# Optimization experiments

Measured on AMD Instinct MI355X. Metric: run time of the kernel, lower is better.

## Reference

```python
import jax, jax.numpy as jnp
import numpy as np

DILATION_RATE = 4
SEGMENT_SIZE = 512


def setup_inputs() -> dict:
    key = jax.random.key(0)
    x = jax.random.normal(key, (4, 8192, 1024), dtype=jnp.float32)
    return {"x": x}


def reference(x):
    """LongNet-style dilated attention.

    For each offset in range(dilation_rate): take the strided slice
    x[:, offset::r, :], split it into segments of length `segment_size`,
    run full softmax(q k^T / sqrt(d)) v attention inside each segment
    (q=k=v=the slice; attention dim is the full d_model, matching how the
    original feeds [B, n_seg, seg, d_model] to FlashAttention), scatter the
    result back to the strided positions, and average the dilation heads
    (softmax over uniform logits == 1/r weights).

    Since seq_len % (r * segment_size) == 0, the r strided slices tile the
    sequence exactly, so we vectorize over offsets with a single reshape:
    position p = i*r + offset  ->  xr[:, i, offset, :].
    """
    r, seg = DILATION_RATE, SEGMENT_SIZE
    B, S, D = x.shape
    n = S // r            # tokens per strided slice
    g = n // seg          # segments per slice
    scale = 1.0 / jnp.sqrt(jnp.asarray(D, dtype=x.dtype))

    xs = x.reshape(B, g, seg, r, D)  # [B, g, seg, r, D]; axis r = dilation offset
    # segment-local attention, independently per (batch, offset, segment)
    scores = jnp.einsum("bgqrd,bgkrd->brgqk", xs, xs) * scale  # [B, r, g, seg, seg]
    probs = jax.nn.softmax(scores, axis=-1)
    out = jnp.einsum("brgqk,bgkrd->bgqrd", probs, xs)          # [B, g, seg, r, D]
    # scatter back to strided positions (pure reshape, since slices tile S),
    # then weighted sum with uniform softmax weights == divide by r.
    return out.reshape(B, S, D) / r
```

## Files before the change

kernel.cpp:

```cpp
#include <hip/hip_runtime.h>
#include <stdint.h>

typedef __bf16 bf16x8  __attribute__((ext_vector_type(8)));
typedef float  f32x4   __attribute__((ext_vector_type(4)));

#define LOG2E    1.44269504088896340736f
#define SM_SCALE 0.03125f

typedef __attribute__((address_space(1))) const uint32_t gau32;
typedef __attribute__((address_space(3))) uint32_t       lau32;
#define GLD16(g, l) __builtin_amdgcn_global_load_lds((gau32*)(g), (lau32*)(l), 16, 0, 0)

__device__ __forceinline__ uint32_t f2bf(float f) {
  uint32_t u = __builtin_bit_cast(uint32_t, f);
  u += 0x7FFFu + ((u >> 16) & 1u);
  return u >> 16;
}
__device__ __forceinline__ uint32_t pk2(float a, float b) {
  return f2bf(a) | (f2bf(b) << 16);
}
__device__ __forceinline__ uint4 pack8(float4 a, float4 b) {
  uint4 r;
  r.x = pk2(a.x, a.y); r.y = pk2(a.z, a.w);
  r.z = pk2(b.x, b.y); r.w = pk2(b.z, b.w);
  return r;
}

__global__ __launch_bounds__(256)
void prep_comb(const float* __restrict__ x, uint16_t* __restrict__ vt,
               uint16_t* __restrict__ xf) {
  __shared__ char tl[64 * 144];
  const int t    = threadIdx.x;
  const int blk  = blockIdx.x;
  const int dc   = blk & 15;
  const int kb   = (blk >> 4) & 7;
  const int prob = blk >> 7;
  const int b  = prob >> 4, off = (prob >> 2) & 3, gs = prob & 3;

  const int key = t >> 2, dq = t & 3;
  const float* src = x + ((size_t)(b * 8192 + gs * 2048 + (kb * 64 + key) * 4 + off)) * 1024
                     + dc * 64 + dq * 16;
  float4 f0 = *(const float4*)(src);
  float4 f1 = *(const float4*)(src + 4);
  float4 f2 = *(const float4*)(src + 8);
  float4 f3 = *(const float4*)(src + 12);
  const int swz = (key & 7) << 4;
  *(uint4*)(tl + key * 144 + ((dq * 32) ^ swz))      = pack8(f0, f1);
  *(uint4*)(tl + key * 144 + ((dq * 32 + 16) ^ swz)) = pack8(f2, f3);
  __syncthreads();
  {
    const int d = t >> 2, kq = t & 3;
    uint32_t w[8];
#pragma unroll
    for (int i = 0; i < 8; ++i) {
      int k0 = kq * 16 + 2 * i, k1 = k0 + 1;
      uint32_t a  = *(const uint16_t*)(tl + k0 * 144 + ((2 * d) ^ ((k0 & 7) << 4)));
      uint32_t bb = *(const uint16_t*)(tl + k1 * 144 + ((2 * d) ^ ((k1 & 7) << 4)));
      w[i] = a | (bb << 16);
    }
    uint16_t* dst = vt + ((size_t)(prob * 1024 + dc * 64 + d)) * 512 + kb * 64 + kq * 16;
    *(uint4*)(dst)     = *(uint4*)&w[0];
    *(uint4*)(dst + 8) = *(uint4*)&w[4];
  }
  {
    const int row = t >> 2, p = t & 3;
    const int dcl = p >> 1;
    const int dq8b = (p & 1) * 2;
    const int swz2 = (row & 7) << 4;
    char* fbase = (char*)xf +
        (((size_t)(prob * 32 + kb * 4 + (row >> 4)) * 32) + (dc * 2 + dcl)) * 1024;
#pragma unroll
    for (int i = 0; i < 2; ++i) {
      const int dq8 = dq8b + i;
      uint4 w = *(const uint4*)(tl + row * 144 + ((dcl * 64 + dq8 * 16) ^ swz2));
      *(uint4*)(fbase + ((row & 15) + 16 * dq8) * 16) = w;
    }
  }
}

#define R6_0 131072
#define R6_1 135168
#define LDS6_BYTES 139264

#define LOADA6(dc, A0, A1) do {                                  \
    A0 = *(const bf16x8*)(xfA0 + (dc) * 1024);                   \
    A1 = *(const bf16x8*)(xfA1 + (dc) * 1024); } while (0)

#define LOADB6(dc, B) do {                                                        \
    const char* qb_ = smem + ((dc) >> 4) * 65536 + ((dc) & 15) * 4096 + lane16;   \
    B[0] = *(const bf16x8*)(qb_);                                                 \
    B[1] = *(const bf16x8*)(qb_ + 1024);                                          \
    B[2] = *(const bf16x8*)(qb_ + 2048);                                          \
    B[3] = *(const bf16x8*)(qb_ + 3072); } while (0)

#define MFMA8(A0, A1, B) do {                                                     \
    S[0][0] = __builtin_amdgcn_mfma_f32_16x16x32_bf16(A0, B[0], S[0][0], 0, 0, 0);\
    S[0][1] = __builtin_amdgcn_mfma_f32_16x16x32_bf16(A0, B[1], S[0][1], 0, 0, 0);\
    S[0][2] = __builtin_amdgcn_mfma_f32_16x16x32_bf16(A0, B[2], S[0][2], 0, 0, 0);\
    S[0][3] = __builtin_amdgcn_mfma_f32_16x16x32_bf16(A0, B[3], S[0][3], 0, 0, 0);\
    S[1][0] = __builtin_amdgcn_mfma_f32_16x16x32_bf16(A1, B[0], S[1][0], 0, 0, 0);\
    S[1][1] = __builtin_amdgcn_mfma_f32_16x16x32_bf16(A1, B[1], S[1][1], 0, 0, 0);\
    S[1][2] = __builtin_amdgcn_mfma_f32_16x16x32_bf16(A1, B[2], S[1][2], 0, 0, 0);\
    S[1][3] = __builtin_amdgcn_mfma_f32_16x16x32_bf16(A1, B[3], S[1][3], 0, 0, 0);\
  } while (0)

__global__ __launch_bounds__(1024, 4)
void dilattn6(const char* __restrict__ xf, const char* __restrict__ vt,
              float* __restrict__ out) {
  extern __shared__ char smem[];

  const int tid  = threadIdx.x;
  const int lane = tid & 63;
  const int wid  = tid >> 6;
  const int h    = lane >> 4;
  const int l15  = lane & 15;
  const int lane16 = lane * 16;

  const int blk  = blockIdx.x;
  const int prob = ((blk & 7) << 3) | (blk >> 6);
  const int q0   = ((blk >> 3) & 7) * 64;
  const int b    = prob >> 4;
  const int off  = (prob >> 2) & 3;
  const int gs   = prob & 3;

  const char* xfp = xf + (size_t)prob * 1048576;
  const int qtile0 = q0 >> 4;

#pragma unroll
  for (int half = 0; half < 2; ++half)
#pragma unroll
    for (int i = 0; i < 4; ++i) {
      const int c = wid * 4 + i;
      const int dcl = c >> 2, qt = c & 3;
      const char* src = xfp + ((size_t)(qtile0 + qt) * 32 + (half * 16 + dcl)) * 1024 + lane16;
      GLD16(src, smem + half * 65536 + dcl * 4096 + qt * 1024);
    }

  const char* xfA0 = xfp + (size_t)(2 * wid) * 32768 + lane16;
  const char* xfA1 = xfA0 + 32768;

  f32x4 S[2][4];
#pragma unroll
  for (int i = 0; i < 2; ++i)
#pragma unroll
    for (int j = 0; j < 4; ++j) S[i][j] = (f32x4){0.f, 0.f, 0.f, 0.f};

  bf16x8 aP0, aP1, aQ0, aQ1, bA[4], bB[4];
  LOADA6(0, aP0, aP1);
  LOADA6(1, aQ0, aQ1);
  __syncthreads();
  LOADB6(0, bA);
  LOADB6(1, bB);

#pragma unroll
  for (int dc2 = 0; dc2 < 32; dc2 += 2) {
    __builtin_amdgcn_s_setprio(1);
    MFMA8(aP0, aP1, bA);
    __builtin_amdgcn_s_setprio(0);
    if (dc2 + 2 < 32) { LOADA6(dc2 + 2, aP0, aP1); LOADB6(dc2 + 2, bA); }
    __builtin_amdgcn_s_setprio(1);
    MFMA8(aQ0, aQ1, bB);
    __builtin_amdgcn_s_setprio(0);
    if (dc2 + 3 < 32) { LOADA6(dc2 + 3, aQ0, aQ1); LOADB6(dc2 + 3, bB); }
  }

  float mq[4], sq[4], rinv[4];
#pragma unroll
  for (int qt = 0; qt < 4; ++qt) {
    float m = S[0][qt][0];
#pragma unroll
    for (int kt = 0; kt < 2; ++kt)
#pragma unroll
      for (int r = 0; r < 4; ++r) m = fmaxf(m, S[kt][qt][r]);
    m = fmaxf(m, __shfl_xor(m, 16, 64));
    m = fmaxf(m, __shfl_xor(m, 32, 64));
    mq[qt] = m;
  }
  if (h == 0) {
#pragma unroll
    for (int qt = 0; qt < 4; ++qt)
      *(float*)(smem + R6_0 + (wid * 64 + 16 * qt + l15) * 4) = mq[qt];
  }
  __syncthreads();
#pragma unroll
  for (int qt = 0; qt < 4; ++qt) {
    float m = -3e38f;
#pragma unroll
    for (int w = 0; w < 16; ++w)
      m = fmaxf(m, *(const float*)(smem + R6_0 + (w * 64 + 16 * qt + l15) * 4));
    mq[qt] = m * SM_SCALE;
    sq[qt] = 0.f;
  }
#pragma unroll
  for (int kt = 0; kt < 2; ++kt)
#pragma unroll
    for (int qt = 0; qt < 4; ++qt)
#pragma unroll
      for (int r = 0; r < 4; ++r) {
        float v = exp2f((S[kt][qt][r] * SM_SCALE - mq[qt]) * LOG2E);
        S[kt][qt][r] = v;
        sq[qt] += v;
      }
#pragma unroll
  for (int qt = 0; qt < 4; ++qt) {
    sq[qt] += __shfl_xor(sq[qt], 16, 64);
    sq[qt] += __shfl_xor(sq[qt], 32, 64);
  }
  if (h == 0) {
#pragma unroll
    for (int qt = 0; qt < 4; ++qt)
      *(float*)(smem + R6_1 + (wid * 64 + 16 * qt + l15) * 4) = sq[qt];
  }
  __syncthreads();
#pragma unroll
  for (int qt = 0; qt < 4; ++qt) {
    float l = 0.f;
#pragma unroll
    for (int w = 0; w < 16; ++w)
      l += *(const float*)(smem + R6_1 + (w * 64 + 16 * qt + l15) * 4);
    rinv[qt] = 0.25f / l;
  }
#pragma unroll
  for (int kt = 0; kt < 2; ++kt)
#pragma unroll
    for (int qt = 0; qt < 4; ++qt) {
      uint2 w2;
      w2.x = pk2(S[kt][qt][0] * rinv[qt], S[kt][qt][1] * rinv[qt]);
      w2.y = pk2(S[kt][qt][2] * rinv[qt], S[kt][qt][3] * rinv[qt]);
      *(uint2*)(smem + qt * 16384 + wid * 1024 +
                (l15 + 16 * (2 * kt + (h >> 1))) * 16 + 8 * (h & 1)) = w2;
    }
  __syncthreads();

  f32x4 acc[4][4];
#pragma unroll
  for (int i = 0; i < 4; ++i)
#pragma unroll
    for (int j = 0; j < 4; ++j) acc[i][j] = (f32x4){0.f, 0.f, 0.f, 0.f};

  const char* vtW = vt + (size_t)prob * 1048576 + (size_t)(64 * wid + l15) * 1024 + 16 * h;

#pragma unroll 2
  for (int ks = 0; ks < 16; ++ks) {
    bf16x8 pa[4];
#pragma unroll
    for (int qt = 0; qt < 4; ++qt)
      pa[qt] = *(const bf16x8*)(smem + qt * 16384 + ks * 1024 + lane16);
    bf16x8 v0 = *(const bf16x8*)(vtW + 0 * 16384 + ks * 64);
    bf16x8 v1 = *(const bf16x8*)(vtW + 1 * 16384 + ks * 64);
    bf16x8 v2 = *(const bf16x8*)(vtW + 2 * 16384 + ks * 64);
    bf16x8 v3 = *(const bf16x8*)(vtW + 3 * 16384 + ks * 64);
    __builtin_amdgcn_s_setprio(1);
#pragma unroll
    for (int qt = 0; qt < 4; ++qt) {
      acc[0][qt] = __builtin_amdgcn_mfma_f32_16x16x32_bf16(pa[qt], v0, acc[0][qt], 0, 0, 0);
      acc[1][qt] = __builtin_amdgcn_mfma_f32_16x16x32_bf16(pa[qt], v1, acc[1][qt], 0, 0, 0);
      acc[2][qt] = __builtin_amdgcn_mfma_f32_16x16x32_bf16(pa[qt], v2, acc[2][qt], 0, 0, 0);
      acc[3][qt] = __builtin_amdgcn_mfma_f32_16x16x32_bf16(pa[qt], v3, acc[3][qt], 0, 0, 0);
    }
    __builtin_amdgcn_s_setprio(0);
  }

  float* outW = out + ((size_t)(b * 8192 + gs * 2048 + (q0 + 4 * h) * 4 + off)) * 1024
                + 64 * wid + l15;
#pragma unroll
  for (int cd = 0; cd < 4; ++cd)
#pragma unroll
    for (int qt = 0; qt < 4; ++qt)
#pragma unroll
      for (int r = 0; r < 4; ++r)
        outW[(size_t)((16 * qt + r) * 4) * 1024 + cd * 16] = acc[cd][qt][r];
}

#define KP_OFF 0
#define Q_OFF  65536
#define RED0   65536
#define RED1   67584
#define LDS_BYTES 73728

__global__ __launch_bounds__(256)
void vt_prepass(const float* __restrict__ x, uint16_t* __restrict__ vt) {
  __shared__ char tl[64 * 144];
  const int t    = threadIdx.x;
  const int blk  = blockIdx.x;
  const int dc   = blk & 15;
  const int kb   = (blk >> 4) & 7;
  const int prob = blk >> 7;
  const int b  = prob >> 4, off = (prob >> 2) & 3, gs = prob & 3;

  const int key = t >> 2, dq = t & 3;
  const float* src = x + ((size_t)(b * 8192 + gs * 2048 + (kb * 64 + key) * 4 + off)) * 1024
                     + dc * 64 + dq * 16;
  float4 f0 = *(const float4*)(src);
  float4 f1 = *(const float4*)(src + 4);
  float4 f2 = *(const float4*)(src + 8);
  float4 f3 = *(const float4*)(src + 12);
  const int swz = (key & 7) << 4;
  *(uint4*)(tl + key * 144 + ((dq * 32) ^ swz))      = pack8(f0, f1);
  *(uint4*)(tl + key * 144 + ((dq * 32 + 16) ^ swz)) = pack8(f2, f3);
  __syncthreads();
  const int d = t >> 2, kq = t & 3;
  uint32_t w[8];
#pragma unroll
  for (int i = 0; i < 8; ++i) {
    int k0 = kq * 16 + 2 * i, k1 = k0 + 1;
    uint32_t a  = *(const uint16_t*)(tl + k0 * 144 + ((2 * d) ^ ((k0 & 7) << 4)));
    uint32_t bb = *(const uint16_t*)(tl + k1 * 144 + ((2 * d) ^ ((k1 & 7) << 4)));
    w[i] = a | (bb << 16);
  }
  uint16_t* dst = vt + ((size_t)(prob * 1024 + dc * 64 + d)) * 512 + kb * 64 + kq * 16;
  *(uint4*)(dst)     = *(uint4*)&w[0];
  *(uint4*)(dst + 8) = *(uint4*)&w[4];
}

template <int USE_VT>
__global__ __launch_bounds__(512, 2)
void dilattn2(const float* __restrict__ x, const uint16_t* __restrict__ vt,
              float* __restrict__ out) {
  extern __shared__ char smem[];

  const int tid  = threadIdx.x;
  const int lane = tid & 63;
  const int wid  = tid >> 6;
  const int h    = lane >> 4;
  const int l15  = lane & 15;
  const int psw  = (l15 & 7) << 4;

  const int blk  = blockIdx.x;
  const int prob = blk >> 3;
  const int q0   = (blk & 7) * 64;
  const int b    = prob >> 4;
  const int off  = (prob >> 2) & 3;
  const int gs   = prob & 3;

  const float* xb = x + (size_t)b * (8192u * 1024u);

  const int srow = tid >> 3;
  const int sg   = tid & 7;
  const float* gK = xb + (size_t)(gs * 2048 + srow * 4 + off) * 1024 + sg * 8;
  const float* gQ = xb + (size_t)(gs * 2048 + (q0 + srow) * 4 + off) * 1024 + sg * 8;
  const int kWr = srow * 128 + ((sg * 16) ^ ((srow & 7) << 4));
  const int qWr = Q_OFF + kWr;

  const int akR = (64 * wid + l15) * 128;
  const int bqR = Q_OFF + l15 * 128;
  const int fb0 = (16 * h) ^ psw;

  f32x4 S[4][4];
#pragma unroll
  for (int i = 0; i < 4; ++i)
#pragma unroll
    for (int j = 0; j < 4; ++j) S[i][j] = (f32x4){0.f, 0.f, 0.f, 0.f};

  float4 kp[16], qp[2];
#pragma unroll
  for (int j = 0; j < 8; ++j) {
    const float* p = gK + (size_t)j * 262144;
    kp[2 * j]     = *(const float4*)(p);
    kp[2 * j + 1] = *(const float4*)(p + 4);
  }
  qp[0] = *(const float4*)(gQ);
  qp[1] = *(const float4*)(gQ + 4);

#pragma unroll 1
  for (int dc = 0; dc < 16; ++dc) {
#pragma unroll
    for (int j = 0; j < 8; ++j)
      *(uint4*)(smem + KP_OFF + kWr + j * 8192) = pack8(kp[2 * j], kp[2 * j + 1]);
    *(uint4*)(smem + qWr) = pack8(qp[0], qp[1]);
    if (dc < 15) {
      const int doff = (dc + 1) * 64;
#pragma unroll
      for (int j = 0; j < 8; ++j) {
        const float* p = gK + (size_t)j * 262144 + doff;
        kp[2 * j]     = *(const float4*)(p);
        kp[2 * j + 1] = *(const float4*)(p + 4);
      }
      qp[0] = *(const float4*)(gQ + doff);
      qp[1] = *(const float4*)(gQ + doff + 4);
    }
    __syncthreads();
#pragma unroll
    for (int s = 0; s < 2; ++s) {
      const int fb = fb0 ^ (s << 6);
      bf16x8 aK[4], bq[4];
#pragma unroll
      for (int kt = 0; kt < 4; ++kt)
        aK[kt] = *(const bf16x8*)(smem + akR + kt * 2048 + fb);
#pragma unroll
      for (int qt = 0; qt < 4; ++qt)
        bq[qt] = *(const bf16x8*)(smem + bqR + qt * 2048 + fb);
#pragma unroll
      for (int kt = 0; kt < 4; ++kt)
#pragma unroll
        for (int qt = 0; qt < 4; ++qt)
          S[kt][qt] = __builtin_amdgcn_mfma_f32_16x16x32_bf16(aK[kt], bq[qt], S[kt][qt], 0, 0, 0);
    }
    __syncthreads();
  }

  float mq[4], sq[4], rinv[4];
#pragma unroll
  for (int qt = 0; qt < 4; ++qt) {
    float m = S[0][qt][0];
#pragma unroll
    for (int kt = 0; kt < 4; ++kt)
#pragma unroll
      for (int r = 0; r < 4; ++r) m = fmaxf(m, S[kt][qt][r]);
    m = fmaxf(m, __shfl_xor(m, 16, 64));
    m = fmaxf(m, __shfl_xor(m, 32, 64));
    mq[qt] = m;
  }
  if (h == 0) {
#pragma unroll
    for (int qt = 0; qt < 4; ++qt)
      *(float*)(smem + RED0 + (wid * 64 + 16 * qt + l15) * 4) = mq[qt];
  }
  __syncthreads();
#pragma unroll
  for (int qt = 0; qt < 4; ++qt) {
    float m = -3e38f;
#pragma unroll
    for (int w = 0; w < 8; ++w)
      m = fmaxf(m, *(const float*)(smem + RED0 + (w * 64 + 16 * qt + l15) * 4));
    mq[qt] = m * SM_SCALE;
    sq[qt] = 0.f;
  }
#pragma unroll
  for (int kt = 0; kt < 4; ++kt)
#pragma unroll
    for (int qt = 0; qt < 4; ++qt)
#pragma unroll
      for (int r = 0; r < 4; ++r) {
        float v = exp2f((S[kt][qt][r] * SM_SCALE - mq[qt]) * LOG2E);
        S[kt][qt][r] = v;
        sq[qt] += v;
      }
#pragma unroll
  for (int qt = 0; qt < 4; ++qt) {
    sq[qt] += __shfl_xor(sq[qt], 16, 64);
    sq[qt] += __shfl_xor(sq[qt], 32, 64);
  }
  if (h == 0) {
#pragma unroll
    for (int qt = 0; qt < 4; ++qt)
      *(float*)(smem + RED1 + (wid * 64 + 16 * qt + l15) * 4) = sq[qt];
  }
  __syncthreads();
#pragma unroll
  for (int qt = 0; qt < 4; ++qt) {
    float l = 0.f;
#pragma unroll
    for (int w = 0; w < 8; ++w)
      l += *(const float*)(smem + RED1 + (w * 64 + 16 * qt + l15) * 4);
    rinv[qt] = 0.25f / l;
  }
#pragma unroll
  for (int kt = 0; kt < 4; ++kt)
#pragma unroll
    for (int qt = 0; qt < 4; ++qt) {
      uint2 w2;
      w2.x = pk2(S[kt][qt][0] * rinv[qt], S[kt][qt][1] * rinv[qt]);
      w2.y = pk2(S[kt][qt][2] * rinv[qt], S[kt][qt][3] * rinv[qt]);
      *(uint2*)(smem + KP_OFF + (16 * qt + l15) * 1024 +
                ((128 * wid + 32 * kt + 8 * h) ^ psw)) = w2;
    }
  __syncthreads();

  f32x4 acc[8][4];
#pragma unroll
  for (int i = 0; i < 8; ++i)
#pragma unroll
    for (int j = 0; j < 4; ++j) acc[i][j] = (f32x4){0.f, 0.f, 0.f, 0.f};

  const uint16_t* vtW = nullptr;
  if constexpr (USE_VT)
    vtW = vt + ((size_t)(prob * 1024 + 128 * wid + l15)) * 512 + 8 * h;

#pragma unroll 1
  for (int ks = 0; ks < 16; ++ks) {
    bf16x8 pa[4];
#pragma unroll
    for (int qt = 0; qt < 4; ++qt)
      pa[qt] = *(const bf16x8*)(smem + KP_OFF + (16 * qt + l15) * 1024 +
                                ((64 * ks + 16 * h) ^ psw));
#pragma unroll
    for (int cd = 0; cd < 8; ++cd) {
      bf16x8 v;
      if constexpr (USE_VT) {
        v = *(const bf16x8*)(vtW + (size_t)((cd >> 2) * 64 + (cd & 3) * 16) * 512 + 32 * ks);
      } else {
        const int d = 128 * wid + (cd >> 2) * 64 + (cd & 3) * 16 + l15;
        union { bf16x8 v; uint16_t u[8]; } a0;
#pragma unroll
        for (int jj = 0; jj < 8; ++jj) {
          int key = 32 * ks + 8 * h + jj;
          a0.u[jj] = (uint16_t)f2bf(xb[(size_t)(gs * 2048 + key * 4 + off) * 1024 + d]);
        }
        v = a0.v;
      }
#pragma unroll
      for (int qt = 0; qt < 4; ++qt)
        acc[cd][qt] = __builtin_amdgcn_mfma_f32_16x16x32_bf16(pa[qt], v, acc[cd][qt], 0, 0, 0);
    }
  }

#pragma unroll
  for (int cd = 0; cd < 8; ++cd) {
    const int d = 128 * wid + (cd >> 2) * 64 + (cd & 3) * 16 + l15;
#pragma unroll
    for (int qt = 0; qt < 4; ++qt)
#pragma unroll
      for (int r = 0; r < 4; ++r) {
        const int qq = q0 + 16 * qt + 4 * h + r;
        out[((size_t)(b * 8192 + gs * 2048 + qq * 4 + off)) * 1024 + d] = acc[cd][qt][r];
      }
  }
}

extern "C" void kernel_launch(void* const* d_in, const int* in_sizes, int n_in,
                              void* d_out, int out_size, void* d_ws, size_t ws_size,
                              hipStream_t stream) {
  const float* x = (const float*)d_in[0];
  float* out = (float*)d_out;
  (void)in_sizes; (void)n_in; (void)out_size;
  const size_t vt_bytes = 64ull * 1024 * 512 * 2;
  const size_t xf_bytes = 64ull * 1024 * 1024;
  if (ws_size >= vt_bytes + xf_bytes) {
    uint16_t* vtp = (uint16_t*)d_ws;
    uint16_t* xfp = (uint16_t*)((char*)d_ws + vt_bytes);
    hipFuncSetAttribute(reinterpret_cast<const void*>(dilattn6),
                        hipFuncAttributeMaxDynamicSharedMemorySize, LDS6_BYTES);
    prep_comb<<<8192, 256, 0, stream>>>(x, vtp, xfp);
    dilattn6<<<512, 1024, LDS6_BYTES, stream>>>((const char*)xfp, (const char*)vtp, out);
  } else if (ws_size >= vt_bytes) {
    uint16_t* vtp = (uint16_t*)d_ws;
    hipFuncSetAttribute(reinterpret_cast<const void*>(dilattn2<1>),
                        hipFuncAttributeMaxDynamicSharedMemorySize, LDS_BYTES);
    vt_prepass<<<8192, 256, 0, stream>>>(x, vtp);
    dilattn2<1><<<512, 512, LDS_BYTES, stream>>>(x, vtp, out);
  } else {
    hipFuncSetAttribute(reinterpret_cast<const void*>(dilattn2<0>),
                        hipFuncAttributeMaxDynamicSharedMemorySize, LDS_BYTES);
    dilattn2<0><<<512, 512, LDS_BYTES, stream>>>(x, nullptr, out);
  }
}
```

Baseline: 190.1 us.

## Stream K and V operands through LDS with async global-to-LDS double buffering

The attention kernel now brings the K-side (A) operands and the V tiles into per-wave LDS double buffers with global_load_lds, instead of loading them straight into registers. The wait on each buffer is set by explicit vmcnt counts, and V prefetch is issued before the softmax phase so it overlaps the reductions. Q staging is split into two 64KB halves that reuse the same LDS region. Block-wide __syncthreads are replaced by lgkmcnt(0) waits plus a raw s_barrier. The goal is to hide global load latency behind MFMA work and to free registers, at the cost of hand-counted wait logic that is easy to get wrong.

```diff
diff --git a/kernel.cpp b/kernel.cpp
--- a/kernel.cpp
+++ b/kernel.cpp
@@ -10,6 +10,12 @@
 typedef __attribute__((address_space(1))) const uint32_t gau32;
 typedef __attribute__((address_space(3))) uint32_t       lau32;
 #define GLD16(g, l) __builtin_amdgcn_global_load_lds((gau32*)(g), (lau32*)(l), 16, 0, 0)
+
+#define VMW2() asm volatile("s_waitcnt vmcnt(2)" ::: "memory")
+#define VMW0() asm volatile("s_waitcnt vmcnt(0)" ::: "memory")
+#define VMW4() asm volatile("s_waitcnt vmcnt(4)" ::: "memory")
+#define LGKM_BAR() do { asm volatile("s_waitcnt lgkmcnt(0)" ::: "memory"); \
+  __builtin_amdgcn_s_barrier(); asm volatile("" ::: "memory"); } while (0)
 
 __device__ __forceinline__ uint32_t f2bf(float f) {
   uint32_t u = __builtin_bit_cast(uint32_t, f);
@@ -78,34 +84,12 @@
   }
 }
 
-#define R6_0 131072
-#define R6_1 135168
-#define LDS6_BYTES 139264
-
-#define LOADA6(dc, A0, A1) do {                                  \
-    A0 = *(const bf16x8*)(xfA0 + (dc) * 1024);                   \
-    A1 = *(const bf16x8*)(xfA1 + (dc) * 1024); } while (0)
-
-#define LOADB6(dc, B) do {                                                        \
-    const char* qb_ = smem + ((dc) >> 4) * 65536 + ((dc) & 15) * 4096 + lane16;   \
-    B[0] = *(const bf16x8*)(qb_);                                                 \
-    B[1] = *(const bf16x8*)(qb_ + 1024);                                          \
-    B[2] = *(const bf16x8*)(qb_ + 2048);                                          \
-    B[3] = *(const bf16x8*)(qb_ + 3072); } while (0)
-
-#define MFMA8(A0, A1, B) do {                                                     \
-    S[0][0] = __builtin_amdgcn_mfma_f32_16x16x32_bf16(A0, B[0], S[0][0], 0, 0, 0);\
-    S[0][1] = __builtin_amdgcn_mfma_f32_16x16x32_bf16(A0, B[1], S[0][1], 0, 0, 0);\
-    S[0][2] = __builtin_amdgcn_mfma_f32_16x16x32_bf16(A0, B[2], S[0][2], 0, 0, 0);\
-    S[0][3] = __builtin_amdgcn_mfma_f32_16x16x32_bf16(A0, B[3], S[0][3], 0, 0, 0);\
-    S[1][0] = __builtin_amdgcn_mfma_f32_16x16x32_bf16(A1, B[0], S[1][0], 0, 0, 0);\
-    S[1][1] = __builtin_amdgcn_mfma_f32_16x16x32_bf16(A1, B[1], S[1][1], 0, 0, 0);\
-    S[1][2] = __builtin_amdgcn_mfma_f32_16x16x32_bf16(A1, B[2], S[1][2], 0, 0, 0);\
-    S[1][3] = __builtin_amdgcn_mfma_f32_16x16x32_bf16(A1, B[3], S[1][3], 0, 0, 0);\
-  } while (0)
+#define R7_0 131072
+#define R7_1 135168
+#define LDS7_BYTES 139264
 
 __global__ __launch_bounds__(1024, 4)
-void dilattn6(const char* __restrict__ xf, const char* __restrict__ vt,
+void dilattn7(const char* __restrict__ xf, const char* __restrict__ vt,
               float* __restrict__ out) {
   extern __shared__ char smem[];
 
@@ -125,19 +109,21 @@
 
   const char* xfp = xf + (size_t)prob * 1048576;
   const int qtile0 = q0 >> 4;
-
-#pragma unroll
-  for (int half = 0; half < 2; ++half)
-#pragma unroll
-    for (int i = 0; i < 4; ++i) {
-      const int c = wid * 4 + i;
-      const int dcl = c >> 2, qt = c & 3;
-      const char* src = xfp + ((size_t)(qtile0 + qt) * 32 + (half * 16 + dcl)) * 1024 + lane16;
-      GLD16(src, smem + half * 65536 + dcl * 4096 + qt * 1024);
-    }
-
   const char* xfA0 = xfp + (size_t)(2 * wid) * 32768 + lane16;
   const char* xfA1 = xfA0 + 32768;
+  char* AVw = smem + 65536 + wid * 4096;
+
+#define STAGE_Q(half) do {                                                           \
+    _Pragma("unroll")                                                                \
+    for (int i_ = 0; i_ < 4; ++i_) {                                                 \
+      const int c_ = wid * 4 + i_;                                                   \
+      const int dcl_ = c_ >> 2, qt_ = c_ & 3;                                        \
+      GLD16(xfp + ((size_t)(qtile0 + qt_) * 32 + ((half) * 16 + dcl_)) * 1024 + lane16, \
+            smem + dcl_ * 4096 + qt_ * 1024); } } while (0)
+
+#define ISSUE_A(ca, s) do {                                                          \
+    GLD16(xfA0 + (ca) * 1024, AVw + (s) * 2048);                                     \
+    GLD16(xfA1 + (ca) * 1024, AVw + (s) * 2048 + 1024); } while (0)
 
   f32x4 S[2][4];
 #pragma unroll
@@ -145,24 +131,51 @@
 #pragma unroll
     for (int j = 0; j < 4; ++j) S[i][j] = (f32x4){0.f, 0.f, 0.f, 0.f};
 
-  bf16x8 aP0, aP1, aQ0, aQ1, bA[4], bB[4];
-  LOADA6(0, aP0, aP1);
-  LOADA6(1, aQ0, aQ1);
-  __syncthreads();
-  LOADB6(0, bA);
-  LOADB6(1, bB);
-
-#pragma unroll
-  for (int dc2 = 0; dc2 < 32; dc2 += 2) {
-    __builtin_amdgcn_s_setprio(1);
-    MFMA8(aP0, aP1, bA);
-    __builtin_amdgcn_s_setprio(0);
-    if (dc2 + 2 < 32) { LOADA6(dc2 + 2, aP0, aP1); LOADB6(dc2 + 2, bA); }
-    __builtin_amdgcn_s_setprio(1);
-    MFMA8(aQ0, aQ1, bB);
-    __builtin_amdgcn_s_setprio(0);
-    if (dc2 + 3 < 32) { LOADA6(dc2 + 3, aQ0, aQ1); LOADB6(dc2 + 3, bB); }
-  }
+#define PH1_HALF(base) do {                                                          \
+    _Pragma("unroll")                                                                \
+    for (int c = 0; c < 16; ++c) {                                                   \
+      if (c < 15) { VMW2(); } else { VMW0(); }                                       \
+      const char* av_ = AVw + (c & 1) * 2048 + lane16;                               \
+      bf16x8 a0 = *(const bf16x8*)(av_);                                             \
+      bf16x8 a1 = *(const bf16x8*)(av_ + 1024);                                      \
+      const char* qb_ = smem + c * 4096 + lane16;                                    \
+      bf16x8 b0 = *(const bf16x8*)(qb_);                                             \
+      bf16x8 b1 = *(const bf16x8*)(qb_ + 1024);                                      \
+      bf16x8 b2 = *(const bf16x8*)(qb_ + 2048);                                      \
+      bf16x8 b3 = *(const bf16x8*)(qb_ + 3072);                                      \
+      __builtin_amdgcn_s_setprio(1);                                                 \
+      S[0][0] = __builtin_amdgcn_mfma_f32_16x16x32_bf16(a0, b0, S[0][0], 0, 0, 0);   \
+      S[0][1] = __builtin_amdgcn_mfma_f32_16x16x32_bf16(a0, b1, S[0][1], 0, 0, 0);   \
+      S[0][2] = __builtin_amdgcn_mfma_f32_16x16x32_bf16(a0, b2, S[0][2], 0, 0, 0);   \
+      S[0][3] = __builtin_amdgcn_mfma_f32_16x16x32_bf16(a0, b3, S[0][3], 0, 0, 0);   \
+      S[1][0] = __builtin_amdgcn_mfma_f32_16x16x32_bf16(a1, b0, S[1][0], 0, 0, 0);   \
+      S[1][1] = __builtin_amdgcn_mfma_f32_16x16x32_bf16(a1, b1, S[1][1], 0, 0, 0);   \
+      S[1][2] = __builtin_amdgcn_mfma_f32_16x16x32_bf16(a1, b2, S[1][2], 0, 0, 0);   \
+      S[1][3] = __builtin_amdgcn_mfma_f32_16x16x32_bf16(a1, b3, S[1][3], 0, 0, 0);   \
+      __builtin_amdgcn_s_setprio(0);                                                 \
+      if (c < 14) ISSUE_A((base) + c + 2, c & 1);                                    \
+    } } while (0)
+
+  STAGE_Q(0);
+  ISSUE_A(0, 0); ISSUE_A(1, 1);
+  VMW4();
+  __builtin_amdgcn_s_barrier();
+  asm volatile("" ::: "memory");
+  PH1_HALF(0);
+  LGKM_BAR();
+  STAGE_Q(1);
+  ISSUE_A(16, 0); ISSUE_A(17, 1);
+  VMW4();
+  __builtin_amdgcn_s_barrier();
+  asm volatile("" ::: "memory");
+  PH1_HALF(16);
+
+  const char* vsrc = vt + (size_t)prob * 1048576 + (size_t)(64 * wid + l15) * 1024 + 16 * h;
+#define ISSUE_V(g, s) do {                                                           \
+    const int ks_ = (g) >> 1, jp_ = (g) & 1;                                         \
+    GLD16(vsrc + (2 * jp_) * 16384 + ks_ * 64, AVw + (s) * 2048);                    \
+    GLD16(vsrc + (2 * jp_ + 1) * 16384 + ks_ * 64, AVw + (s) * 2048 + 1024); } while (0)
+  ISSUE_V(0, 0); ISSUE_V(1, 1);
 
   float mq[4], sq[4], rinv[4];
 #pragma unroll
@@ -179,15 +192,15 @@
   if (h == 0) {
 #pragma unroll
     for (int qt = 0; qt < 4; ++qt)
-      *(float*)(smem + R6_0 + (wid * 64 + 16 * qt + l15) * 4) = mq[qt];
-  }
-  __syncthreads();
+      *(float*)(smem + R7_0 + (wid * 64 + 16 * qt + l15) * 4) = mq[qt];
+  }
+  LGKM_BAR();
 #pragma unroll
   for (int qt = 0; qt < 4; ++qt) {
     float m = -3e38f;
 #pragma unroll
     for (int w = 0; w < 16; ++w)
-      m = fmaxf(m, *(const float*)(smem + R6_0 + (w * 64 + 16 * qt + l15) * 4));
+      m = fmaxf(m, *(const float*)(smem + R7_0 + (w * 64 + 16 * qt + l15) * 4));
     mq[qt] = m * SM_SCALE;
     sq[qt] = 0.f;
   }
@@ -209,15 +222,15 @@
   if (h == 0) {
 #pragma unroll
     for (int qt = 0; qt < 4; ++qt)
-      *(float*)(smem + R6_1 + (wid * 64 + 16 * qt + l15) * 4) = sq[qt];
-  }
-  __syncthreads();
+      *(float*)(smem + R7_1 + (wid * 64 + 16 * qt + l15) * 4) = sq[qt];
+  }
+  LGKM_BAR();
 #pragma unroll
   for (int qt = 0; qt < 4; ++qt) {
     float l = 0.f;
 #pragma unroll
     for (int w = 0; w < 16; ++w)
-      l += *(const float*)(smem + R6_1 + (w * 64 + 16 * qt + l15) * 4);
+      l += *(const float*)(smem + R7_1 + (w * 64 + 16 * qt + l15) * 4);
     rinv[qt] = 0.25f / l;
   }
 #pragma unroll
@@ -230,7 +243,7 @@
       *(uint2*)(smem + qt * 16384 + wid * 1024 +
                 (l15 + 16 * (2 * kt + (h >> 1))) * 16 + 8 * (h & 1)) = w2;
     }
-  __syncthreads();
+  LGKM_BAR();
 
   f32x4 acc[4][4];
 #pragma unroll
@@ -238,27 +251,28 @@
 #pragma unroll
     for (int j = 0; j < 4; ++j) acc[i][j] = (f32x4){0.f, 0.f, 0.f, 0.f};
 
-  const char* vtW = vt + (size_t)prob * 1048576 + (size_t)(64 * wid + l15) * 1024 + 16 * h;
-
-#pragma unroll 2
-  for (int ks = 0; ks < 16; ++ks) {
-    bf16x8 pa[4];
-#pragma unroll
-    for (int qt = 0; qt < 4; ++qt)
-      pa[qt] = *(const bf16x8*)(smem + qt * 16384 + ks * 1024 + lane16);
-    bf16x8 v0 = *(const bf16x8*)(vtW + 0 * 16384 + ks * 64);
-    bf16x8 v1 = *(const bf16x8*)(vtW + 1 * 16384 + ks * 64);
-    bf16x8 v2 = *(const bf16x8*)(vtW + 2 * 16384 + ks * 64);
-    bf16x8 v3 = *(const bf16x8*)(vtW + 3 * 16384 + ks * 64);
+  bf16x8 pa[4];
+#pragma unroll
+  for (int g = 0; g < 32; ++g) {
+    if (g < 31) { VMW2(); } else { VMW0(); }
+    if ((g & 1) == 0) {
+      const int ks = g >> 1;
+#pragma unroll
+      for (int qt = 0; qt < 4; ++qt)
+        pa[qt] = *(const bf16x8*)(smem + qt * 16384 + ks * 1024 + lane16);
+    }
+    const char* av = AVw + (g & 1) * 2048 + lane16;
+    bf16x8 va = *(const bf16x8*)(av);
+    bf16x8 vb = *(const bf16x8*)(av + 1024);
+    const int j0 = (g & 1) * 2;
     __builtin_amdgcn_s_setprio(1);
 #pragma unroll
     for (int qt = 0; qt < 4; ++qt) {
-      acc[0][qt] = __builtin_amdgcn_mfma_f32_16x16x32_bf16(pa[qt], v0, acc[0][qt], 0, 0, 0);
-      acc[1][qt] = __builtin_amdgcn_mfma_f32_16x16x32_bf16(pa[qt], v1, acc[1][qt], 0, 0, 0);
-      acc[2][qt] = __builtin_amdgcn_mfma_f32_16x16x32_bf16(pa[qt], v2, acc[2][qt], 0, 0, 0);
-      acc[3][qt] = __builtin_amdgcn_mfma_f32_16x16x32_bf16(pa[qt], v3, acc[3][qt], 0, 0, 0);
+      acc[j0][qt]     = __builtin_amdgcn_mfma_f32_16x16x32_bf16(pa[qt], va, acc[j0][qt], 0, 0, 0);
+      acc[j0 + 1][qt] = __builtin_amdgcn_mfma_f32_16x16x32_bf16(pa[qt], vb, acc[j0 + 1][qt], 0, 0, 0);
     }
     __builtin_amdgcn_s_setprio(0);
+    if (g < 30) ISSUE_V(g + 2, g & 1);
   }
 
   float* outW = out + ((size_t)(b * 8192 + gs * 2048 + (q0 + 4 * h) * 4 + off)) * 1024
@@ -270,6 +284,10 @@
 #pragma unroll
       for (int r = 0; r < 4; ++r)
         outW[(size_t)((16 * qt + r) * 4) * 1024 + cd * 16] = acc[cd][qt][r];
+#undef STAGE_Q
+#undef ISSUE_A
+#undef ISSUE_V
+#undef PH1_HALF
 }
 
 #define KP_OFF 0
@@ -529,10 +547,10 @@
   if (ws_size >= vt_bytes + xf_bytes) {
     uint16_t* vtp = (uint16_t*)d_ws;
     uint16_t* xfp = (uint16_t*)((char*)d_ws + vt_bytes);
-    hipFuncSetAttribute(reinterpret_cast<const void*>(dilattn6),
-                        hipFuncAttributeMaxDynamicSharedMemorySize, LDS6_BYTES);
+    hipFuncSetAttribute(reinterpret_cast<const void*>(dilattn7),
+                        hipFuncAttributeMaxDynamicSharedMemorySize, LDS7_BYTES);
     prep_comb<<<8192, 256, 0, stream>>>(x, vtp, xfp);
-    dilattn6<<<512, 1024, LDS6_BYTES, stream>>>((const char*)xfp, (const char*)vtp, out);
+    dilattn7<<<512, 1024, LDS7_BYTES, stream>>>((const char*)xfp, (const char*)vtp, out);
   } else if (ws_size >= vt_bytes) {
     uint16_t* vtp = (uint16_t*)d_ws;
     hipFuncSetAttribute(reinterpret_cast<const void*>(dilattn2<1>),
```

Result: no change. 189.8 us (-0.2%).

## Double query tile per block to 128 rows, halving grid and K reloads

Applied to the files above, without the earlier changes.

Each block now handles 128 query rows instead of 64, so the key rows each wave streams from global memory are reused across twice as many queries, and the grid shrinks from 512 to 256 blocks. The Q tile is staged through LDS in two halves of the head dimension, with syncs in between, instead of preloading the full tile. The PV stage is split into two passes over the output columns to keep the accumulator count in registers manageable. The cost is fewer blocks than compute units on a 256-CU part, more registers per thread, and the loss of the previous double-buffered software pipelining in the QK loop.

```diff
diff --git a/kernel.cpp b/kernel.cpp
--- a/kernel.cpp
+++ b/kernel.cpp
@@ -78,34 +78,12 @@
   }
 }
 
-#define R6_0 131072
-#define R6_1 135168
-#define LDS6_BYTES 139264
-
-#define LOADA6(dc, A0, A1) do {                                  \
-    A0 = *(const bf16x8*)(xfA0 + (dc) * 1024);                   \
-    A1 = *(const bf16x8*)(xfA1 + (dc) * 1024); } while (0)
-
-#define LOADB6(dc, B) do {                                                        \
-    const char* qb_ = smem + ((dc) >> 4) * 65536 + ((dc) & 15) * 4096 + lane16;   \
-    B[0] = *(const bf16x8*)(qb_);                                                 \
-    B[1] = *(const bf16x8*)(qb_ + 1024);                                          \
-    B[2] = *(const bf16x8*)(qb_ + 2048);                                          \
-    B[3] = *(const bf16x8*)(qb_ + 3072); } while (0)
-
-#define MFMA8(A0, A1, B) do {                                                     \
-    S[0][0] = __builtin_amdgcn_mfma_f32_16x16x32_bf16(A0, B[0], S[0][0], 0, 0, 0);\
-    S[0][1] = __builtin_amdgcn_mfma_f32_16x16x32_bf16(A0, B[1], S[0][1], 0, 0, 0);\
-    S[0][2] = __builtin_amdgcn_mfma_f32_16x16x32_bf16(A0, B[2], S[0][2], 0, 0, 0);\
-    S[0][3] = __builtin_amdgcn_mfma_f32_16x16x32_bf16(A0, B[3], S[0][3], 0, 0, 0);\
-    S[1][0] = __builtin_amdgcn_mfma_f32_16x16x32_bf16(A1, B[0], S[1][0], 0, 0, 0);\
-    S[1][1] = __builtin_amdgcn_mfma_f32_16x16x32_bf16(A1, B[1], S[1][1], 0, 0, 0);\
-    S[1][2] = __builtin_amdgcn_mfma_f32_16x16x32_bf16(A1, B[2], S[1][2], 0, 0, 0);\
-    S[1][3] = __builtin_amdgcn_mfma_f32_16x16x32_bf16(A1, B[3], S[1][3], 0, 0, 0);\
-  } while (0)
+#define R9_0 131072
+#define R9_1 139264
+#define LDS9_BYTES 147456
 
 __global__ __launch_bounds__(1024, 4)
-void dilattn6(const char* __restrict__ xf, const char* __restrict__ vt,
+void dilattn9(const char* __restrict__ xf, const char* __restrict__ vt,
               float* __restrict__ out) {
   extern __shared__ char smem[];
 
@@ -117,56 +95,57 @@
   const int lane16 = lane * 16;
 
   const int blk  = blockIdx.x;
-  const int prob = ((blk & 7) << 3) | (blk >> 6);
-  const int q0   = ((blk >> 3) & 7) * 64;
+  const int jj   = blk >> 3;
+  const int prob = ((blk & 7) << 3) + (jj >> 2);
+  const int q0   = (jj & 3) * 128;
   const int b    = prob >> 4;
   const int off  = (prob >> 2) & 3;
   const int gs   = prob & 3;
 
   const char* xfp = xf + (size_t)prob * 1048576;
   const int qtile0 = q0 >> 4;
-
-#pragma unroll
-  for (int half = 0; half < 2; ++half)
-#pragma unroll
-    for (int i = 0; i < 4; ++i) {
-      const int c = wid * 4 + i;
-      const int dcl = c >> 2, qt = c & 3;
-      const char* src = xfp + ((size_t)(qtile0 + qt) * 32 + (half * 16 + dcl)) * 1024 + lane16;
-      GLD16(src, smem + half * 65536 + dcl * 4096 + qt * 1024);
-    }
-
-  const char* xfA0 = xfp + (size_t)(2 * wid) * 32768 + lane16;
-  const char* xfA1 = xfA0 + 32768;
-
-  f32x4 S[2][4];
+  const char* xfA = xfp + (size_t)(2 * wid) * 32768 + lane16;
+
+  f32x4 S[2][8];
 #pragma unroll
   for (int i = 0; i < 2; ++i)
 #pragma unroll
-    for (int j = 0; j < 4; ++j) S[i][j] = (f32x4){0.f, 0.f, 0.f, 0.f};
-
-  bf16x8 aP0, aP1, aQ0, aQ1, bA[4], bB[4];
-  LOADA6(0, aP0, aP1);
-  LOADA6(1, aQ0, aQ1);
-  __syncthreads();
-  LOADB6(0, bA);
-  LOADB6(1, bB);
-
-#pragma unroll
-  for (int dc2 = 0; dc2 < 32; dc2 += 2) {
-    __builtin_amdgcn_s_setprio(1);
-    MFMA8(aP0, aP1, bA);
-    __builtin_amdgcn_s_setprio(0);
-    if (dc2 + 2 < 32) { LOADA6(dc2 + 2, aP0, aP1); LOADB6(dc2 + 2, bA); }
-    __builtin_amdgcn_s_setprio(1);
-    MFMA8(aQ0, aQ1, bB);
-    __builtin_amdgcn_s_setprio(0);
-    if (dc2 + 3 < 32) { LOADA6(dc2 + 3, aQ0, aQ1); LOADB6(dc2 + 3, bB); }
-  }
-
-  float mq[4], sq[4], rinv[4];
-#pragma unroll
-  for (int qt = 0; qt < 4; ++qt) {
+    for (int j = 0; j < 8; ++j) S[i][j] = (f32x4){0.f, 0.f, 0.f, 0.f};
+
+#pragma unroll 1
+  for (int half = 0; half < 2; ++half) {
+#pragma unroll
+    for (int i = 0; i < 8; ++i) {
+      const int c_ = wid * 8 + i;
+      const int dcl = c_ >> 3, qt = c_ & 7;
+      GLD16(xfp + ((size_t)(qtile0 + qt) * 32 + (half * 16 + dcl)) * 1024 + lane16,
+            smem + dcl * 8192 + qt * 1024);
+    }
+    __syncthreads();
+#pragma unroll
+    for (int dc = 0; dc < 16; ++dc) {
+      const int dca = half * 16 + dc;
+      bf16x8 a0 = *(const bf16x8*)(xfA + dca * 1024);
+      bf16x8 a1 = *(const bf16x8*)(xfA + 32768 + dca * 1024);
+      const char* qb = smem + dc * 8192 + lane16;
+      bf16x8 bq[8];
+#pragma unroll
+      for (int qt = 0; qt < 8; ++qt)
+        bq[qt] = *(const bf16x8*)(qb + qt * 1024);
+      __builtin_amdgcn_s_setprio(1);
+#pragma unroll
+      for (int qt = 0; qt < 8; ++qt) {
+        S[0][qt] = __builtin_amdgcn_mfma_f32_16x16x32_bf16(a0, bq[qt], S[0][qt], 0, 0, 0);
+        S[1][qt] = __builtin_amdgcn_mfma_f32_16x16x32_bf16(a1, bq[qt], S[1][qt], 0, 0, 0);
+      }
+      __builtin_amdgcn_s_setprio(0);
+    }
+    __syncthreads();
+  }
+
+  float mq[8], sq[8], rinv[8];
+#pragma unroll
+  for (int qt = 0; qt < 8; ++qt) {
     float m = S[0][qt][0];
 #pragma unroll
     for (int kt = 0; kt < 2; ++kt)
@@ -178,23 +157,23 @@
   }
   if (h == 0) {
 #pragma unroll
-    for (int qt = 0; qt < 4; ++qt)
-      *(float*)(smem + R6_0 + (wid * 64 + 16 * qt + l15) * 4) = mq[qt];
-  }
-  __syncthreads();
-#pragma unroll
-  for (int qt = 0; qt < 4; ++qt) {
+    for (int qt = 0; qt < 8; ++qt)
+      *(float*)(smem + R9_0 + (wid * 128 + qt * 16 + l15) * 4) = mq[qt];
+  }
+  __syncthreads();
+#pragma unroll
+  for (int qt = 0; qt < 8; ++qt) {
     float m = -3e38f;
 #pragma unroll
     for (int w = 0; w < 16; ++w)
-      m = fmaxf(m, *(const float*)(smem + R6_0 + (w * 64 + 16 * qt + l15) * 4));
+      m = fmaxf(m, *(const float*)(smem + R9_0 + (w * 128 + qt * 16 + l15) * 4));
     mq[qt] = m * SM_SCALE;
     sq[qt] = 0.f;
   }
 #pragma unroll
   for (int kt = 0; kt < 2; ++kt)
 #pragma unroll
-    for (int qt = 0; qt < 4; ++qt)
+    for (int qt = 0; qt < 8; ++qt)
 #pragma unroll
       for (int r = 0; r < 4; ++r) {
         float v = exp2f((S[kt][qt][r] * SM_SCALE - mq[qt]) * LOG2E);
@@ -202,28 +181,28 @@
         sq[qt] += v;
       }
 #pragma unroll
-  for (int qt = 0; qt < 4; ++qt) {
+  for (int qt = 0; qt < 8; ++qt) {
     sq[qt] += __shfl_xor(sq[qt], 16, 64);
     sq[qt] += __shfl_xor(sq[qt], 32, 64);
   }
   if (h == 0) {
 #pragma unroll
-    for (int qt = 0; qt < 4; ++qt)
-      *(float*)(smem + R6_1 + (wid * 64 + 16 * qt + l15) * 4) = sq[qt];
-  }
-  __syncthreads();
-#pragma unroll
-  for (int qt = 0; qt < 4; ++qt) {
+    for (int qt = 0; qt < 8; ++qt)
+      *(float*)(smem + R9_1 + (wid * 128 + qt * 16 + l15) * 4) = sq[qt];
+  }
+  __syncthreads();
+#pragma unroll
+  for (int qt = 0; qt < 8; ++qt) {
     float l = 0.f;
 #pragma unroll
     for (int w = 0; w < 16; ++w)
-      l += *(const float*)(smem + R6_1 + (w * 64 + 16 * qt + l15) * 4);
+      l += *(const float*)(smem + R9_1 + (w * 128 + qt * 16 + l15) * 4);
     rinv[qt] = 0.25f / l;
   }
 #pragma unroll
   for (int kt = 0; kt < 2; ++kt)
 #pragma unroll
-    for (int qt = 0; qt < 4; ++qt) {
+    for (int qt = 0; qt < 8; ++qt) {
       uint2 w2;
       w2.x = pk2(S[kt][qt][0] * rinv[qt], S[kt][qt][1] * rinv[qt]);
       w2.y = pk2(S[kt][qt][2] * rinv[qt], S[kt][qt][3] * rinv[qt]);
@@ -232,44 +211,42 @@
     }
   __syncthreads();
 
-  f32x4 acc[4][4];
-#pragma unroll
-  for (int i = 0; i < 4; ++i)
-#pragma unroll
-    for (int j = 0; j < 4; ++j) acc[i][j] = (f32x4){0.f, 0.f, 0.f, 0.f};
-
-  const char* vtW = vt + (size_t)prob * 1048576 + (size_t)(64 * wid + l15) * 1024 + 16 * h;
-
-#pragma unroll 2
-  for (int ks = 0; ks < 16; ++ks) {
-    bf16x8 pa[4];
-#pragma unroll
-    for (int qt = 0; qt < 4; ++qt)
-      pa[qt] = *(const bf16x8*)(smem + qt * 16384 + ks * 1024 + lane16);
-    bf16x8 v0 = *(const bf16x8*)(vtW + 0 * 16384 + ks * 64);
-    bf16x8 v1 = *(const bf16x8*)(vtW + 1 * 16384 + ks * 64);
-    bf16x8 v2 = *(const bf16x8*)(vtW + 2 * 16384 + ks * 64);
-    bf16x8 v3 = *(const bf16x8*)(vtW + 3 * 16384 + ks * 64);
-    __builtin_amdgcn_s_setprio(1);
-#pragma unroll
-    for (int qt = 0; qt < 4; ++qt) {
-      acc[0][qt] = __builtin_amdgcn_mfma_f32_16x16x32_bf16(pa[qt], v0, acc[0][qt], 0, 0, 0);
-      acc[1][qt] = __builtin_amdgcn_mfma_f32_16x16x32_bf16(pa[qt], v1, acc[1][qt], 0, 0, 0);
-      acc[2][qt] = __builtin_amdgcn_mfma_f32_16x16x32_bf16(pa[qt], v2, acc[2][qt], 0, 0, 0);
-      acc[3][qt] = __builtin_amdgcn_mfma_f32_16x16x32_bf16(pa[qt], v3, acc[3][qt], 0, 0, 0);
-    }
-    __builtin_amdgcn_s_setprio(0);
-  }
-
-  float* outW = out + ((size_t)(b * 8192 + gs * 2048 + (q0 + 4 * h) * 4 + off)) * 1024
-                + 64 * wid + l15;
-#pragma unroll
-  for (int cd = 0; cd < 4; ++cd)
-#pragma unroll
-    for (int qt = 0; qt < 4; ++qt)
-#pragma unroll
-      for (int r = 0; r < 4; ++r)
-        outW[(size_t)((16 * qt + r) * 4) * 1024 + cd * 16] = acc[cd][qt][r];
+#pragma unroll 1
+  for (int p = 0; p < 2; ++p) {
+    const int dbase = p * 512 + 32 * wid;
+    f32x4 acc[2][8];
+#pragma unroll
+    for (int i = 0; i < 2; ++i)
+#pragma unroll
+      for (int j = 0; j < 8; ++j) acc[i][j] = (f32x4){0.f, 0.f, 0.f, 0.f};
+
+    const char* vtW = vt + (size_t)prob * 1048576 + (size_t)(dbase + l15) * 1024 + 16 * h;
+#pragma unroll 1
+    for (int ks = 0; ks < 16; ++ks) {
+      bf16x8 pa[8];
+#pragma unroll
+      for (int qt = 0; qt < 8; ++qt)
+        pa[qt] = *(const bf16x8*)(smem + qt * 16384 + ks * 1024 + lane16);
+      bf16x8 v0 = *(const bf16x8*)(vtW + ks * 64);
+      bf16x8 v1 = *(const bf16x8*)(vtW + 16384 + ks * 64);
+      __builtin_amdgcn_s_setprio(1);
+#pragma unroll
+      for (int qt = 0; qt < 8; ++qt) {
+        acc[0][qt] = __builtin_amdgcn_mfma_f32_16x16x32_bf16(pa[qt], v0, acc[0][qt], 0, 0, 0);
+        acc[1][qt] = __builtin_amdgcn_mfma_f32_16x16x32_bf16(pa[qt], v1, acc[1][qt], 0, 0, 0);
+      }
+      __builtin_amdgcn_s_setprio(0);
+    }
+    float* outW = out + ((size_t)(b * 8192 + gs * 2048 + (q0 + 4 * h) * 4 + off)) * 1024
+                  + dbase + l15;
+#pragma unroll
+    for (int cd = 0; cd < 2; ++cd)
+#pragma unroll
+      for (int qt = 0; qt < 8; ++qt)
+#pragma unroll
+        for (int r = 0; r < 4; ++r)
+          outW[(size_t)((16 * qt + r) * 4) * 1024 + cd * 16] = acc[cd][qt][r];
+  }
 }
 
 #define KP_OFF 0
@@ -529,10 +506,10 @@
   if (ws_size >= vt_bytes + xf_bytes) {
     uint16_t* vtp = (uint16_t*)d_ws;
     uint16_t* xfp = (uint16_t*)((char*)d_ws + vt_bytes);
-    hipFuncSetAttribute(reinterpret_cast<const void*>(dilattn6),
-                        hipFuncAttributeMaxDynamicSharedMemorySize, LDS6_BYTES);
+    hipFuncSetAttribute(reinterpret_cast<const void*>(dilattn9),
+                        hipFuncAttributeMaxDynamicSharedMemorySize, LDS9_BYTES);
     prep_comb<<<8192, 256, 0, stream>>>(x, vtp, xfp);
-    dilattn6<<<512, 1024, LDS6_BYTES, stream>>>((const char*)xfp, (const char*)vtp, out);
+    dilattn9<<<256, 1024, LDS9_BYTES, stream>>>((const char*)xfp, (const char*)vtp, out);
   } else if (ws_size >= vt_bytes) {
     uint16_t* vtp = (uint16_t*)d_ws;
     hipFuncSetAttribute(reinterpret_cast<const void*>(dilattn2<1>),
```

Result: faster. 172.6 us (-9.2%).
